# Performance work log

Measured on AMD Instinct MI355X. Metric: run time of the kernel, lower is better.

The kernel has to match this reference:

```python
import jax, jax.numpy as jnp
import numpy as np

B, N, DIN, DOUT = 64, 1024, 64, 64


def setup_inputs() -> dict:
    key = jax.random.key(0)
    k1, k2, k3 = jax.random.split(key, 3)
    # adj entries in (0,1): positive row-sums so rsqrt(degree) is finite
    adj_batch = jax.random.uniform(k1, (B, N, N), dtype=jnp.float32)
    att_batch = jax.random.normal(k2, (B, N, DIN), dtype=jnp.float32)
    # xavier_uniform_ init for weight
    bound = float(np.sqrt(6.0 / (DIN + DOUT)))
    weight = jax.random.uniform(k3, (DIN, DOUT), dtype=jnp.float32,
                                minval=-bound, maxval=bound)
    return {"adj_batch": adj_batch, "att_batch": att_batch, "weight": weight}


def reference(adj_batch, att_batch, weight):
    # Degrees computed on adj BEFORE self-loops (faithful to the torch code).
    deg = jnp.sum(adj_batch, axis=-1)              # [B, N]
    dinv = jax.lax.rsqrt(deg)                      # 1/sqrt(deg), diag of D
    # s_adj = adj + I  (self-loops added AFTER degree computation)
    s_adj = adj_batch + jnp.eye(N, dtype=adj_batch.dtype)[None]  # [B, N, N]
    # out = D @ s_adj @ D @ (att @ W); diagonal matmuls fused as row scalings
    x = jnp.einsum('bnd,de->bne', att_batch, weight)   # att @ W   [B, N, DOUT]
    x = dinv[..., None] * x                             # D @ x
    y = jnp.einsum('bij,bjd->bid', s_adj, x)            # s_adj @ (D x)
    out = dinv[..., None] * y                           # D @ (...)
    return (out, weight)
```

## Files before the change

### kernel.cpp

```cpp
#include <hip/hip_runtime.h>
#include <stdint.h>
#include <stddef.h>

#define BATCH 64
#define NN    1024
#define DD    64

typedef _Float16 h8 __attribute__((ext_vector_type(8)));
typedef _Float16 h4 __attribute__((ext_vector_type(4)));
typedef float    f32x4 __attribute__((ext_vector_type(4)));

__device__ __forceinline__ int swz(int row, int gran) {
    return (row << 3) + (gran ^ (row & 7));
}

__global__ __launch_bounds__(256) void k_wt(const float* __restrict__ w,
                                            _Float16* __restrict__ wt) {
#pragma unroll
    for (int it = 0; it < 4; ++it) {
        const int idx = threadIdx.x + (it << 8);
        const int k = idx >> 4, d4 = idx & 15;
        const float4 v = ((const float4*)w)[idx];
        wt[(d4 * 4 + 0) * DD + k] = (_Float16)v.x;
        wt[(d4 * 4 + 1) * DD + k] = (_Float16)v.y;
        wt[(d4 * 4 + 2) * DD + k] = (_Float16)v.z;
        wt[(d4 * 4 + 3) * DD + k] = (_Float16)v.w;
    }
}

__global__ __launch_bounds__(256) void k_deg(const float* __restrict__ adj,
                                             _Float16* __restrict__ adjh,
                                             float* __restrict__ dinv,
                                             int writeH) {
    const int lane = threadIdx.x & 63;
    const int rowg = blockIdx.x * 4 + (threadIdx.x >> 6);
    const int i = rowg & (NN - 1);
    const float* rp = adj + (size_t)rowg * NN;
    float s = 0.f;
#pragma unroll
    for (int k = 0; k < 4; ++k) {
        const int f4 = lane + (k << 6);
        const float4 v = ((const float4*)rp)[f4];
        s += v.x + v.y + v.z + v.w;
        if (writeH) {
            const int j0 = f4 << 2;
            h4 o;
            o[0] = (_Float16)(v.x + ((j0 + 0) == i ? 1.f : 0.f));
            o[1] = (_Float16)(v.y + ((j0 + 1) == i ? 1.f : 0.f));
            o[2] = (_Float16)(v.z + ((j0 + 2) == i ? 1.f : 0.f));
            o[3] = (_Float16)(v.w + ((j0 + 3) == i ? 1.f : 0.f));
            ((h4*)(adjh + (size_t)rowg * NN))[f4] = o;
        }
    }
#pragma unroll
    for (int off = 32; off; off >>= 1) s += __shfl_xor(s, off);
    if (lane == 0) dinv[rowg] = 1.f / sqrtf(s);
}

__global__ __launch_bounds__(256) void k_xw(const float* __restrict__ att,
                                            const _Float16* __restrict__ wt,
                                            const float* __restrict__ dinv,
                                            _Float16* __restrict__ zT) {
    __shared__ __align__(16) _Float16 attS[128 * 64];
    __shared__ __align__(16) _Float16 wtS[64 * 64];
    const int t = threadIdx.x;
    const int bb = blockIdx.y;
    const int j0 = blockIdx.x * 128;

#pragma unroll
    for (int it = 0; it < 4; ++it) {
        const int g = t + (it << 8);
        const int r = g >> 3, c = g & 7;
        const float4* p = (const float4*)(att + (size_t)(bb * NN + j0 + r) * DD + (c << 3));
        const float4 v0 = p[0], v1 = p[1];
        h8 o;
        o[0] = (_Float16)v0.x; o[1] = (_Float16)v0.y; o[2] = (_Float16)v0.z; o[3] = (_Float16)v0.w;
        o[4] = (_Float16)v1.x; o[5] = (_Float16)v1.y; o[6] = (_Float16)v1.z; o[7] = (_Float16)v1.w;
        *(h8*)&attS[swz(r, c) * 8] = o;
    }
#pragma unroll
    for (int it = 0; it < 2; ++it) {
        const int g = t + (it << 8);
        const int r = g >> 3, c = g & 7;
        const h8 v = *(const h8*)(wt + r * DD + (c << 3));
        *(h8*)&wtS[swz(r, c) * 8] = v;
    }
    __syncthreads();

    const int w = t >> 6, lane = t & 63;
    const int lr = lane & 15, lg = lane >> 4;
    const f32x4 zero = {0.f, 0.f, 0.f, 0.f};
    f32x4 acc[2][4];
#pragma unroll
    for (int mf = 0; mf < 2; ++mf)
#pragma unroll
        for (int nf = 0; nf < 4; ++nf) acc[mf][nf] = zero;

#pragma unroll
    for (int kk = 0; kk < 2; ++kk) {
        h8 a[2], bfr[4];
#pragma unroll
        for (int mf = 0; mf < 2; ++mf) {
            const int row = w * 32 + mf * 16 + lr;
            a[mf] = *(const h8*)&attS[swz(row, kk * 4 + lg) * 8];
        }
#pragma unroll
        for (int nf = 0; nf < 4; ++nf) {
            const int row = nf * 16 + lr;
            bfr[nf] = *(const h8*)&wtS[swz(row, kk * 4 + lg) * 8];
        }
#pragma unroll
        for (int mf = 0; mf < 2; ++mf)
#pragma unroll
            for (int nf = 0; nf < 4; ++nf)
                acc[mf][nf] = __builtin_amdgcn_mfma_f32_16x16x32_f16(a[mf], bfr[nf], acc[mf][nf], 0, 0, 0);
    }

#pragma unroll
    for (int mf = 0; mf < 2; ++mf) {
        const int jb = j0 + w * 32 + mf * 16 + lg * 4;
        const float4 dv = *(const float4*)&dinv[bb * NN + jb];
#pragma unroll
        for (int nf = 0; nf < 4; ++nf) {
            const int d = nf * 16 + lr;
            h4 o;
            o[0] = (_Float16)(acc[mf][nf][0] * dv.x);
            o[1] = (_Float16)(acc[mf][nf][1] * dv.y);
            o[2] = (_Float16)(acc[mf][nf][2] * dv.z);
            o[3] = (_Float16)(acc[mf][nf][3] * dv.w);
            *(h4*)(zT + (size_t)(bb * DD + d) * NN + jb) = o;
        }
    }
}

template <int FROM_F32>
__global__ __launch_bounds__(256) void k_agg(const _Float16* __restrict__ adjh,
                                             const float* __restrict__ adjf,
                                             const _Float16* __restrict__ zT,
                                             const float* __restrict__ dinv,
                                             float* __restrict__ out) {
    __shared__ __align__(16) _Float16 adjS[64 * 64];
    __shared__ __align__(16) _Float16 zS[64 * 64];
    const int t = threadIdx.x;
    const int bb = blockIdx.y;
    const int i0 = blockIdx.x * 64;
    const int w = t >> 6, lane = t & 63;
    const int lr = lane & 15, lg = lane >> 4;
    const f32x4 zero = {0.f, 0.f, 0.f, 0.f};
    f32x4 acc[4];
#pragma unroll
    for (int nf = 0; nf < 4; ++nf) acc[nf] = zero;

    for (int kt = 0; kt < 16; ++kt) {
        __syncthreads();
#pragma unroll
        for (int it = 0; it < 2; ++it) {
            const int g = t + (it << 8);
            const int r = g >> 3, c = g & 7;
            if constexpr (FROM_F32) {
                const int gj = kt * 64 + (c << 3);
                const int gi = i0 + r;
                const float4* p = (const float4*)(adjf + (size_t)(bb * NN + gi) * NN + gj);
                const float4 v0 = p[0], v1 = p[1];
                h8 o;
                o[0] = (_Float16)(v0.x + ((gj + 0) == gi ? 1.f : 0.f));
                o[1] = (_Float16)(v0.y + ((gj + 1) == gi ? 1.f : 0.f));
                o[2] = (_Float16)(v0.z + ((gj + 2) == gi ? 1.f : 0.f));
                o[3] = (_Float16)(v0.w + ((gj + 3) == gi ? 1.f : 0.f));
                o[4] = (_Float16)(v1.x + ((gj + 4) == gi ? 1.f : 0.f));
                o[5] = (_Float16)(v1.y + ((gj + 5) == gi ? 1.f : 0.f));
                o[6] = (_Float16)(v1.z + ((gj + 6) == gi ? 1.f : 0.f));
                o[7] = (_Float16)(v1.w + ((gj + 7) == gi ? 1.f : 0.f));
                *(h8*)&adjS[swz(r, c) * 8] = o;
            } else {
                const h8 v = *(const h8*)(adjh + (size_t)(bb * NN + i0 + r) * NN + kt * 64 + (c << 3));
                *(h8*)&adjS[swz(r, c) * 8] = v;
            }
            const h8 vz = *(const h8*)(zT + (size_t)(bb * DD + r) * NN + kt * 64 + (c << 3));
            *(h8*)&zS[swz(r, c) * 8] = vz;
        }
        __syncthreads();
#pragma unroll
        for (int kk = 0; kk < 2; ++kk) {
            const h8 a = *(const h8*)&adjS[swz(w * 16 + lr, kk * 4 + lg) * 8];
#pragma unroll
            for (int nf = 0; nf < 4; ++nf) {
                const h8 bz = *(const h8*)&zS[swz(nf * 16 + lr, kk * 4 + lg) * 8];
                acc[nf] = __builtin_amdgcn_mfma_f32_16x16x32_f16(a, bz, acc[nf], 0, 0, 0);
            }
        }
    }

    const int ib = i0 + w * 16 + lg * 4;
    const float4 dv = *(const float4*)&dinv[bb * NN + ib];
#pragma unroll
    for (int nf = 0; nf < 4; ++nf) {
        const int d = nf * 16 + lr;
        float* op = out + (size_t)(bb * NN + ib) * DD + d;
        op[0 * DD] = acc[nf][0] * dv.x;
        op[1 * DD] = acc[nf][1] * dv.y;
        op[2 * DD] = acc[nf][2] * dv.z;
        op[3 * DD] = acc[nf][3] * dv.w;
    }
}

__global__ __launch_bounds__(256) void k_wcopy(const float* __restrict__ w,
                                               float* __restrict__ ow) {
#pragma unroll
    for (int it = 0; it < 4; ++it) {
        const int idx = threadIdx.x + (it << 8);
        ((float4*)ow)[idx] = ((const float4*)w)[idx];
    }
}

extern "C" void kernel_launch(void* const* d_in, const int* in_sizes, int n_in,
                              void* d_out, int out_size, void* d_ws, size_t ws_size,
                              hipStream_t stream) {
    const float* adj = (const float*)d_in[0];
    const float* att = (const float*)d_in[1];
    const float* wgt = (const float*)d_in[2];
    float* out = (float*)d_out;
    char* ws = (char*)d_ws;

    const size_t adjh_bytes = (size_t)BATCH * NN * NN * 2;
    const size_t z_bytes    = (size_t)BATCH * DD * NN * 2;
    const size_t dinv_bytes = (size_t)BATCH * NN * 4;
    const size_t wt_bytes   = (size_t)DD * DD * 2;
    const bool planA = ws_size >= adjh_bytes + z_bytes + dinv_bytes + wt_bytes;

    size_t off = 0;
    _Float16* adjh = nullptr;
    if (planA) { adjh = (_Float16*)ws; off += adjh_bytes; }
    _Float16* zT  = (_Float16*)(ws + off); off += z_bytes;
    float*    dinv = (float*)(ws + off);   off += dinv_bytes;
    _Float16* wt  = (_Float16*)(ws + off);

    k_wt<<<1, 256, 0, stream>>>(wgt, wt);
    k_deg<<<BATCH * NN / 4, 256, 0, stream>>>(adj, adjh, dinv, planA ? 1 : 0);
    k_xw<<<dim3(NN / 128, BATCH), 256, 0, stream>>>(att, wt, dinv, zT);
    if (planA)
        k_agg<0><<<dim3(NN / 64, BATCH), 256, 0, stream>>>(adjh, nullptr, zT, dinv, out);
    else
        k_agg<1><<<dim3(NN / 64, BATCH), 256, 0, stream>>>(nullptr, adj, zT, dinv, out);
    k_wcopy<<<1, 256, 0, stream>>>(wgt, out + (size_t)BATCH * NN * DD);
}
```

Measured before the change: 119.5 us.

## Drop fp16 adjacency copy, scale adj columns by dinv in aggregation, prefetch tiles

Removes the materialized fp16 adjacency (written by the degree kernel and read back by aggregation). The aggregation now reads fp32 adj directly, multiplies each column by dinv[j] while converting to fp16, and adds the self-loop term on the diagonal tile; k_xw no longer applies dinv. It also adds register prefetch of the next tile to overlap global loads with MFMA, and folds the weight copy into k_wt. This cuts a 128MB write plus a 128MB read but makes aggregation read adj in fp32 twice overall (deg plus agg).

```diff
diff --git a/kernel.cpp b/kernel.cpp
--- a/kernel.cpp
+++ b/kernel.cpp
@@ -15,7 +15,8 @@
 }
 
 __global__ __launch_bounds__(256) void k_wt(const float* __restrict__ w,
-                                            _Float16* __restrict__ wt) {
+                                            _Float16* __restrict__ wt,
+                                            float* __restrict__ ow) {
 #pragma unroll
     for (int it = 0; it < 4; ++it) {
         const int idx = threadIdx.x + (it << 8);
@@ -25,41 +26,12 @@
         wt[(d4 * 4 + 1) * DD + k] = (_Float16)v.y;
         wt[(d4 * 4 + 2) * DD + k] = (_Float16)v.z;
         wt[(d4 * 4 + 3) * DD + k] = (_Float16)v.w;
-    }
-}
-
-__global__ __launch_bounds__(256) void k_deg(const float* __restrict__ adj,
-                                             _Float16* __restrict__ adjh,
-                                             float* __restrict__ dinv,
-                                             int writeH) {
-    const int lane = threadIdx.x & 63;
-    const int rowg = blockIdx.x * 4 + (threadIdx.x >> 6);
-    const int i = rowg & (NN - 1);
-    const float* rp = adj + (size_t)rowg * NN;
-    float s = 0.f;
-#pragma unroll
-    for (int k = 0; k < 4; ++k) {
-        const int f4 = lane + (k << 6);
-        const float4 v = ((const float4*)rp)[f4];
-        s += v.x + v.y + v.z + v.w;
-        if (writeH) {
-            const int j0 = f4 << 2;
-            h4 o;
-            o[0] = (_Float16)(v.x + ((j0 + 0) == i ? 1.f : 0.f));
-            o[1] = (_Float16)(v.y + ((j0 + 1) == i ? 1.f : 0.f));
-            o[2] = (_Float16)(v.z + ((j0 + 2) == i ? 1.f : 0.f));
-            o[3] = (_Float16)(v.w + ((j0 + 3) == i ? 1.f : 0.f));
-            ((h4*)(adjh + (size_t)rowg * NN))[f4] = o;
-        }
-    }
-#pragma unroll
-    for (int off = 32; off; off >>= 1) s += __shfl_xor(s, off);
-    if (lane == 0) dinv[rowg] = 1.f / sqrtf(s);
+        ((float4*)ow)[idx] = v;
+    }
 }
 
 __global__ __launch_bounds__(256) void k_xw(const float* __restrict__ att,
                                             const _Float16* __restrict__ wt,
-                                            const float* __restrict__ dinv,
                                             _Float16* __restrict__ zT) {
     __shared__ __align__(16) _Float16 attS[128 * 64];
     __shared__ __align__(16) _Float16 wtS[64 * 64];
@@ -100,15 +72,11 @@
     for (int kk = 0; kk < 2; ++kk) {
         h8 a[2], bfr[4];
 #pragma unroll
-        for (int mf = 0; mf < 2; ++mf) {
-            const int row = w * 32 + mf * 16 + lr;
-            a[mf] = *(const h8*)&attS[swz(row, kk * 4 + lg) * 8];
-        }
-#pragma unroll
-        for (int nf = 0; nf < 4; ++nf) {
-            const int row = nf * 16 + lr;
-            bfr[nf] = *(const h8*)&wtS[swz(row, kk * 4 + lg) * 8];
-        }
+        for (int mf = 0; mf < 2; ++mf)
+            a[mf] = *(const h8*)&attS[swz(w * 32 + mf * 16 + lr, kk * 4 + lg) * 8];
+#pragma unroll
+        for (int nf = 0; nf < 4; ++nf)
+            bfr[nf] = *(const h8*)&wtS[swz(nf * 16 + lr, kk * 4 + lg) * 8];
 #pragma unroll
         for (int mf = 0; mf < 2; ++mf)
 #pragma unroll
@@ -119,23 +87,36 @@
 #pragma unroll
     for (int mf = 0; mf < 2; ++mf) {
         const int jb = j0 + w * 32 + mf * 16 + lg * 4;
-        const float4 dv = *(const float4*)&dinv[bb * NN + jb];
 #pragma unroll
         for (int nf = 0; nf < 4; ++nf) {
             const int d = nf * 16 + lr;
             h4 o;
-            o[0] = (_Float16)(acc[mf][nf][0] * dv.x);
-            o[1] = (_Float16)(acc[mf][nf][1] * dv.y);
-            o[2] = (_Float16)(acc[mf][nf][2] * dv.z);
-            o[3] = (_Float16)(acc[mf][nf][3] * dv.w);
+            o[0] = (_Float16)acc[mf][nf][0];
+            o[1] = (_Float16)acc[mf][nf][1];
+            o[2] = (_Float16)acc[mf][nf][2];
+            o[3] = (_Float16)acc[mf][nf][3];
             *(h4*)(zT + (size_t)(bb * DD + d) * NN + jb) = o;
         }
     }
 }
 
-template <int FROM_F32>
-__global__ __launch_bounds__(256) void k_agg(const _Float16* __restrict__ adjh,
-                                             const float* __restrict__ adjf,
+__global__ __launch_bounds__(256) void k_deg(const float* __restrict__ adj,
+                                             float* __restrict__ dinv) {
+    const int lane = threadIdx.x & 63;
+    const int rowg = blockIdx.x * 4 + (threadIdx.x >> 6);
+    const float* rp = adj + (size_t)rowg * NN;
+    float s = 0.f;
+#pragma unroll
+    for (int k = 0; k < 4; ++k) {
+        const float4 v = ((const float4*)rp)[lane + (k << 6)];
+        s += v.x + v.y + v.z + v.w;
+    }
+#pragma unroll
+    for (int off = 32; off; off >>= 1) s += __shfl_xor(s, off);
+    if (lane == 0) dinv[rowg] = 1.f / sqrtf(s);
+}
+
+__global__ __launch_bounds__(256) void k_agg(const float* __restrict__ adj,
                                              const _Float16* __restrict__ zT,
                                              const float* __restrict__ dinv,
                                              float* __restrict__ out) {
@@ -146,40 +127,63 @@
     const int i0 = blockIdx.x * 64;
     const int w = t >> 6, lane = t & 63;
     const int lr = lane & 15, lg = lane >> 4;
+    const float* dvB = dinv + bb * NN;
+    const int ktDiag = i0 >> 6;
+
+    const int r0 = t >> 3, c0 = t & 7;
+    const int r1 = (t + 256) >> 3, c1 = t & 7;
+
+    float4 pa[2][2];
+    float4 pd[2][2];
+    h8     pz[2];
+
+    auto loadT = [&](int kt) {
+        const int gj0 = kt * 64 + (c0 << 3);
+        const float4* p0 = (const float4*)(adj + (size_t)(bb * NN + i0 + r0) * NN + gj0);
+        pa[0][0] = p0[0]; pa[0][1] = p0[1];
+        pd[0][0] = *(const float4*)(dvB + gj0);
+        pd[0][1] = *(const float4*)(dvB + gj0 + 4);
+        pz[0] = *(const h8*)(zT + (size_t)(bb * DD + r0) * NN + gj0);
+        const int gj1 = kt * 64 + (c1 << 3);
+        const float4* p1 = (const float4*)(adj + (size_t)(bb * NN + i0 + r1) * NN + gj1);
+        pa[1][0] = p1[0]; pa[1][1] = p1[1];
+        pd[1][0] = *(const float4*)(dvB + gj1);
+        pd[1][1] = *(const float4*)(dvB + gj1 + 4);
+        pz[1] = *(const h8*)(zT + (size_t)(bb * DD + r1) * NN + gj1);
+    };
+    auto writeT = [&]() {
+#pragma unroll
+        for (int it = 0; it < 2; ++it) {
+            const int r = it ? r1 : r0, c = it ? c1 : c0;
+            h8 o;
+            o[0] = (_Float16)(pa[it][0].x * pd[it][0].x);
+            o[1] = (_Float16)(pa[it][0].y * pd[it][0].y);
+            o[2] = (_Float16)(pa[it][0].z * pd[it][0].z);
+            o[3] = (_Float16)(pa[it][0].w * pd[it][0].w);
+            o[4] = (_Float16)(pa[it][1].x * pd[it][1].x);
+            o[5] = (_Float16)(pa[it][1].y * pd[it][1].y);
+            o[6] = (_Float16)(pa[it][1].z * pd[it][1].z);
+            o[7] = (_Float16)(pa[it][1].w * pd[it][1].w);
+            *(h8*)&adjS[swz(r, c) * 8] = o;
+            *(h8*)&zS[swz(r, c) * 8] = pz[it];
+        }
+    };
+
     const f32x4 zero = {0.f, 0.f, 0.f, 0.f};
     f32x4 acc[4];
 #pragma unroll
     for (int nf = 0; nf < 4; ++nf) acc[nf] = zero;
 
+    loadT(0);
     for (int kt = 0; kt < 16; ++kt) {
+        writeT();
+        if (kt == ktDiag) {
+            __syncthreads();
+            if (t < 64)
+                adjS[swz(t, t >> 3) * 8 + (t & 7)] += (_Float16)dvB[i0 + t];
+        }
         __syncthreads();
-#pragma unroll
-        for (int it = 0; it < 2; ++it) {
-            const int g = t + (it << 8);
-            const int r = g >> 3, c = g & 7;
-            if constexpr (FROM_F32) {
-                const int gj = kt * 64 + (c << 3);
-                const int gi = i0 + r;
-                const float4* p = (const float4*)(adjf + (size_t)(bb * NN + gi) * NN + gj);
-                const float4 v0 = p[0], v1 = p[1];
-                h8 o;
-                o[0] = (_Float16)(v0.x + ((gj + 0) == gi ? 1.f : 0.f));
-                o[1] = (_Float16)(v0.y + ((gj + 1) == gi ? 1.f : 0.f));
-                o[2] = (_Float16)(v0.z + ((gj + 2) == gi ? 1.f : 0.f));
-                o[3] = (_Float16)(v0.w + ((gj + 3) == gi ? 1.f : 0.f));
-                o[4] = (_Float16)(v1.x + ((gj + 4) == gi ? 1.f : 0.f));
-                o[5] = (_Float16)(v1.y + ((gj + 5) == gi ? 1.f : 0.f));
-                o[6] = (_Float16)(v1.z + ((gj + 6) == gi ? 1.f : 0.f));
-                o[7] = (_Float16)(v1.w + ((gj + 7) == gi ? 1.f : 0.f));
-                *(h8*)&adjS[swz(r, c) * 8] = o;
-            } else {
-                const h8 v = *(const h8*)(adjh + (size_t)(bb * NN + i0 + r) * NN + kt * 64 + (c << 3));
-                *(h8*)&adjS[swz(r, c) * 8] = v;
-            }
-            const h8 vz = *(const h8*)(zT + (size_t)(bb * DD + r) * NN + kt * 64 + (c << 3));
-            *(h8*)&zS[swz(r, c) * 8] = vz;
-        }
-        __syncthreads();
+        if (kt < 15) loadT(kt + 1);
 #pragma unroll
         for (int kk = 0; kk < 2; ++kk) {
             const h8 a = *(const h8*)&adjS[swz(w * 16 + lr, kk * 4 + lg) * 8];
@@ -189,6 +193,7 @@
                 acc[nf] = __builtin_amdgcn_mfma_f32_16x16x32_f16(a, bz, acc[nf], 0, 0, 0);
             }
         }
+        __syncthreads();
     }
 
     const int ib = i0 + w * 16 + lg * 4;
@@ -201,15 +206,6 @@
         op[1 * DD] = acc[nf][1] * dv.y;
         op[2 * DD] = acc[nf][2] * dv.z;
         op[3 * DD] = acc[nf][3] * dv.w;
-    }
-}
-
-__global__ __launch_bounds__(256) void k_wcopy(const float* __restrict__ w,
-                                               float* __restrict__ ow) {
-#pragma unroll
-    for (int it = 0; it < 4; ++it) {
-        const int idx = threadIdx.x + (it << 8);
-        ((float4*)ow)[idx] = ((const float4*)w)[idx];
     }
 }
 
@@ -222,25 +218,13 @@
     float* out = (float*)d_out;
     char* ws = (char*)d_ws;
 
-    const size_t adjh_bytes = (size_t)BATCH * NN * NN * 2;
-    const size_t z_bytes    = (size_t)BATCH * DD * NN * 2;
-    const size_t dinv_bytes = (size_t)BATCH * NN * 4;
-    const size_t wt_bytes   = (size_t)DD * DD * 2;
-    const bool planA = ws_size >= adjh_bytes + z_bytes + dinv_bytes + wt_bytes;
-
     size_t off = 0;
-    _Float16* adjh = nullptr;
-    if (planA) { adjh = (_Float16*)ws; off += adjh_bytes; }
-    _Float16* zT  = (_Float16*)(ws + off); off += z_bytes;
-    float*    dinv = (float*)(ws + off);   off += dinv_bytes;
+    _Float16* zT  = (_Float16*)(ws + off); off += (size_t)BATCH * DD * NN * 2;
+    float*    dinv = (float*)(ws + off);   off += (size_t)BATCH * NN * 4;
     _Float16* wt  = (_Float16*)(ws + off);
 
-    k_wt<<<1, 256, 0, stream>>>(wgt, wt);
-    k_deg<<<BATCH * NN / 4, 256, 0, stream>>>(adj, adjh, dinv, planA ? 1 : 0);
-    k_xw<<<dim3(NN / 128, BATCH), 256, 0, stream>>>(att, wt, dinv, zT);
-    if (planA)
-        k_agg<0><<<dim3(NN / 64, BATCH), 256, 0, stream>>>(adjh, nullptr, zT, dinv, out);
-    else
-        k_agg<1><<<dim3(NN / 64, BATCH), 256, 0, stream>>>(nullptr, adj, zT, dinv, out);
-    k_wcopy<<<1, 256, 0, stream>>>(wgt, out + (size_t)BATCH * NN * DD);
-}
+    k_wt<<<1, 256, 0, stream>>>(wgt, wt, out + (size_t)BATCH * NN * DD);
+    k_xw<<<dim3(NN / 128, BATCH), 256, 0, stream>>>(att, wt, zT);
+    k_deg<<<BATCH * NN / 4, 256, 0, stream>>>(adj, dinv);
+    k_agg<<<dim3(NN / 64, BATCH), 256, 0, stream>>>(adj, zT, dinv, out);
+}
```

Measured after the change: 109.1 us. 1.1x faster.
